# Kernel tuning notes

Measured on AMD Instinct MI355X. Metric: run time of the kernel, lower is better.

Reference implementation:

```python
import jax, jax.numpy as jnp
import numpy as np

B, N, T, D, H, E = 2, 1024, 8, 128, 4, 8192
DH = D // H
NEG_SLOPE = 0.2  # GATv2Conv default negative_slope


def _ln(x, g, b):
    m = jnp.mean(x, -1, keepdims=True)
    v = jnp.mean((x - m) ** 2, -1, keepdims=True)
    return (x - m) * jax.lax.rsqrt(v + 1e-5) * g + b


def _forward(x, edge_index, gat_wl, gat_wr, gat_att, gat_b, in_w, in_b, out_w, out_b,
             ffn_w1, ffn_b1, ffn_w2, ffn_b2, fus_w, fus_b,
             lns_g, lns_b, lnt1_g, lnt1_b, lnt2_g, lnt2_b, lnf_g, lnf_b):
    # ---- spatial branch: GATv2, vectorized over (B, T) instead of python loops ----
    loops = jnp.arange(N)
    src = jnp.concatenate([edge_index[0], loops])  # j: message source (PyG adds self loops)
    dst = jnp.concatenate([edge_index[1], loops])  # i: aggregation target
    xl = jnp.einsum('bntd,de->bnte', x, gat_wl).reshape(B, N, T, H, D)
    xr = jnp.einsum('bntd,de->bnte', x, gat_wr).reshape(B, N, T, H, D)
    ml = xl[:, src]                                  # [B,Et,T,H,D]
    mr = xr[:, dst]
    e = jax.nn.leaky_relu(ml + mr, NEG_SLOPE)
    logits = jnp.einsum('bethd,hd->beth', e, gat_att)
    logits = jnp.moveaxis(logits, 1, 0)              # [Et,B,T,H]
    mx = jax.ops.segment_max(logits, dst, num_segments=N)
    p = jnp.exp(logits - mx[dst])                    # stable edge softmax per dst node
    ssum = jax.ops.segment_sum(p, dst, num_segments=N)
    alpha = p / ssum[dst]                            # [Et,B,T,H]
    msg = alpha[..., None] * jnp.moveaxis(ml, 1, 0)
    agg = jax.ops.segment_sum(msg, dst, num_segments=N)  # [N,B,T,H,D]
    x_sp = jnp.moveaxis(agg.mean(3), 0, 1) + gat_b   # concat=False -> head mean; [B,N,T,D]
    x_sp = _ln(x_sp, lns_g, lns_b)

    # ---- temporal branch: MHA + FFN, vectorized over all B*N nodes ----
    xt = x.reshape(B * N, T, D)
    qkv = xt @ in_w + in_b
    q, k, v = jnp.split(qkv, 3, axis=-1)
    q = q.reshape(B * N, T, H, DH)
    k = k.reshape(B * N, T, H, DH)
    v = v.reshape(B * N, T, H, DH)
    scores = jnp.einsum('bthd,bshd->bhts', q, k) / np.float32(np.sqrt(DH))
    attn = jax.nn.softmax(scores, -1)
    o = jnp.einsum('bhts,bshd->bthd', attn, v).reshape(B * N, T, D)
    o = o @ out_w + out_b
    x1 = _ln(xt + o, lnt1_g, lnt1_b)
    ffn = jax.nn.gelu(x1 @ ffn_w1 + ffn_b1, approximate=False) @ ffn_w2 + ffn_b2
    x_tp = _ln(x1 + ffn, lnt2_g, lnt2_b).reshape(B, N, T, D)

    # ---- gated fusion with residual ----
    g = jax.nn.sigmoid(jnp.concatenate([x_sp, x_tp], -1) @ fus_w + fus_b)
    return _ln(g * x_sp + (1.0 - g) * x_tp + x, lnf_g, lnf_b)


def setup_inputs() -> dict:
    key = jax.random.key(0)
    ks = jax.random.split(key, 12)
    s = 0.05
    f = jnp.float32
    return {
        'x': jax.random.normal(ks[0], (B, N, T, D), f),
        'edge_index': jax.random.randint(ks[1], (2, E), 0, N),
        'gat_wl': jax.random.normal(ks[2], (D, H * D), f) * s,
        'gat_wr': jax.random.normal(ks[3], (D, H * D), f) * s,
        'gat_att': jax.random.normal(ks[4], (H, D), f) * s,
        'gat_b': jnp.zeros((D,), f),
        'in_w': jax.random.normal(ks[5], (D, 3 * D), f) * s,
        'in_b': jnp.zeros((3 * D,), f),
        'out_w': jax.random.normal(ks[6], (D, D), f) * s,
        'out_b': jnp.zeros((D,), f),
        'ffn_w1': jax.random.normal(ks[7], (D, 4 * D), f) * s,
        'ffn_b1': jnp.zeros((4 * D,), f),
        'ffn_w2': jax.random.normal(ks[8], (4 * D, D), f) * s,
        'ffn_b2': jnp.zeros((D,), f),
        'fus_w': jax.random.normal(ks[9], (2 * D, D), f) * s,
        'fus_b': jnp.zeros((D,), f),
        'lns_g': jnp.ones((D,), f), 'lns_b': jnp.zeros((D,), f),
        'lnt1_g': jnp.ones((D,), f), 'lnt1_b': jnp.zeros((D,), f),
        'lnt2_g': jnp.ones((D,), f), 'lnt2_b': jnp.zeros((D,), f),
        'lnf_g': jnp.ones((D,), f), 'lnf_b': jnp.zeros((D,), f),
    }


def reference(x, edge_index, gat_wl, gat_wr, gat_att, gat_b, in_w, in_b, out_w, out_b,
              ffn_w1, ffn_b1, ffn_w2, ffn_b2, fus_w, fus_b,
              lns_g, lns_b, lnt1_g, lnt1_b, lnt2_g, lnt2_b, lnf_g, lnf_b):
    return _forward(x, edge_index, gat_wl, gat_wr, gat_att, gat_b, in_w, in_b, out_w, out_b,
                    ffn_w1, ffn_b1, ffn_w2, ffn_b2, fus_w, fus_b,
                    lns_g, lns_b, lnt1_g, lnt1_b, lnt2_g, lnt2_b, lnf_g, lnf_b)
```

## Files before the change

### kernel.cpp

```cpp
#include <hip/hip_runtime.h>
#include <math.h>

#define B_ 2
#define N_ 1024
#define T_ 8
#define D_ 128
#define H_ 4
#define E_ 8192
#define EN_ 9216
#define M_ 16384

typedef unsigned short u16;
using bf16x8 = __attribute__((ext_vector_type(8))) short;
using f32x4  = __attribute__((ext_vector_type(4))) float;

__device__ __forceinline__ float bf2f(unsigned int u) {
  return __uint_as_float(u << 16);
}
__device__ __forceinline__ u16 f2bf(float f) {
  unsigned int x = __float_as_uint(f);
  x += 0x7fffu + ((x >> 16) & 1u);
  return (u16)(x >> 16);
}
__device__ __forceinline__ void load8f(const u16* p, float* f) {
  uint4 u = *(const uint4*)p;
  f[0]=bf2f(u.x & 0xffffu); f[1]=bf2f(u.x >> 16);
  f[2]=bf2f(u.y & 0xffffu); f[3]=bf2f(u.y >> 16);
  f[4]=bf2f(u.z & 0xffffu); f[5]=bf2f(u.z >> 16);
  f[6]=bf2f(u.w & 0xffffu); f[7]=bf2f(u.w >> 16);
}
__device__ __forceinline__ void unpack8(uint4 u, float* f) {
  f[0]=bf2f(u.x & 0xffffu); f[1]=bf2f(u.x >> 16);
  f[2]=bf2f(u.y & 0xffffu); f[3]=bf2f(u.y >> 16);
  f[4]=bf2f(u.z & 0xffffu); f[5]=bf2f(u.z >> 16);
  f[6]=bf2f(u.w & 0xffffu); f[7]=bf2f(u.w >> 16);
}
__device__ __forceinline__ void gl2lds(const u16* g, u16* l) {
  __builtin_amdgcn_global_load_lds(
      (const __attribute__((address_space(1))) unsigned int*)(const void*)g,
      (__attribute__((address_space(3))) unsigned int*)(void*)l,
      16, 0, 0);
}

__device__ __forceinline__ u16 conv_w_elem(int idx,
    const float* wl, const float* wr, const float* inw, const float* outw,
    const float* f1, const float* f2, const float* fw) {
  const float* src; int base, K, N;
  if      (idx < 65536)  { src = wl;   base = 0;      K = 128; N = 512; }
  else if (idx < 131072) { src = wr;   base = 65536;  K = 128; N = 512; }
  else if (idx < 180224) { src = inw;  base = 131072; K = 128; N = 384; }
  else if (idx < 196608) { src = outw; base = 180224; K = 128; N = 128; }
  else if (idx < 262144) { src = f1;   base = 196608; K = 128; N = 512; }
  else if (idx < 327680) { src = f2;   base = 262144; K = 512; N = 128; }
  else                   { src = fw;   base = 327680; K = 256; N = 128; }
  int o = idx - base;
  int n = o / K, k = o - n * K;
  return f2bf(src[k * N + n]);
}

__global__ __launch_bounds__(1024) void prep_csr_k(const float* __restrict__ x,
    const float* __restrict__ wl, const float* __restrict__ wr,
    const float* __restrict__ inw, const float* __restrict__ outw,
    const float* __restrict__ f1, const float* __restrict__ f2,
    const float* __restrict__ fw,
    u16* __restrict__ XB, u16* __restrict__ WB,
    const int* __restrict__ ei, int* __restrict__ offs, int* __restrict__ srcs) {
  __shared__ int cnt[N_];
  __shared__ int cur[N_];
  int bi = blockIdx.x;
  int tid = threadIdx.x;
  if (bi < 512) {
    int i = (bi * 1024 + tid) * 4;
    float4 v = *(const float4*)&x[i];
    u16 o[4] = {f2bf(v.x), f2bf(v.y), f2bf(v.z), f2bf(v.w)};
    *(ushort4*)&XB[i] = *(ushort4*)o;
    return;
  }
  if (bi < 600) {
    int base = (bi - 512) * 4096 + tid * 4;
#pragma unroll
    for (int j = 0; j < 4; ++j)
      WB[base + j] = conv_w_elem(base + j, wl, wr, inw, outw, f1, f2, fw);
    return;
  }
  cnt[tid] = 0;
  __syncthreads();
  for (int e = tid; e < EN_; e += 1024) {
    int d = (e < E_) ? ei[E_ + e] : (e - E_);
    atomicAdd(&cnt[d], 1);
  }
  __syncthreads();
  int mine = cnt[tid];
  for (int off = 1; off < 1024; off <<= 1) {
    int tv = (tid >= off) ? cnt[tid - off] : 0;
    __syncthreads();
    cnt[tid] += tv;
    __syncthreads();
  }
  int excl = cnt[tid] - mine;
  offs[tid] = excl;
  if (tid == 1023) offs[N_] = cnt[1023];
  cur[tid] = excl;
  __syncthreads();
  for (int e = tid; e < EN_; e += 1024) {
    int d = (e < E_) ? ei[E_ + e] : (e - E_);
    int s = (e < E_) ? ei[e] : (e - E_);
    int pos = atomicAdd(&cur[d], 1);
    srcs[pos] = s;
  }
}

template<int BM, int ACT, int ROUTE>
__global__ __launch_bounds__(256) void gemm_k(const u16* __restrict__ A, int lda,
                                              const u16* __restrict__ WT, int K,
                                              const float* __restrict__ bias,
                                              u16* __restrict__ C, int ldc,
                                              u16* __restrict__ R0,
                                              u16* __restrict__ R1,
                                              u16* __restrict__ R2,
                                              const float* __restrict__ b2) {
  constexpr int MI = BM / 32;
  __shared__ u16 As[BM * 32];
  __shared__ u16 Bs[128 * 32];
  int tid = threadIdx.x;
  int bx = blockIdx.x, by = blockIdx.y;
  int lane = tid & 63, wid = tid >> 6;
  int lr = lane & 15, lk = lane >> 4;
  int wm = (wid >> 1) * (BM / 2);
  int wn = (wid & 1) * 64;

  u16* Cb; int ldc_; int col0; const float* bias_;
  if (ROUTE) {
    if (bx < 4)      { Cb = R0; ldc_ = 512; col0 = bx * 128;       bias_ = nullptr; }
    else if (bx < 8) { Cb = R1; ldc_ = 512; col0 = (bx - 4) * 128; bias_ = nullptr; }
    else             { Cb = R2; ldc_ = 384; col0 = (bx - 8) * 128; bias_ = b2; }
  } else { Cb = C; ldc_ = ldc; col0 = bx * 128; bias_ = bias; }

  f32x4 acc[MI][4] = {};
  for (int k0 = 0; k0 < K; k0 += 32) {
    __syncthreads();
#pragma unroll
    for (int i = 0; i < BM / 64; ++i) {
      int o = tid * 16 + i * 4096;
      int row = o >> 6;
      int col = (o >> 1) & 31;
      gl2lds(A + (size_t)(by * BM + row) * lda + k0 + col,
             (u16*)((char*)As + wid * 1024 + i * 4096));
    }
#pragma unroll
    for (int i = 0; i < 2; ++i) {
      int o = tid * 16 + i * 4096;
      int nrow = o >> 6;
      int col = (o >> 1) & 31;
      gl2lds(WT + (size_t)(bx * 128 + nrow) * K + k0 + col,
             (u16*)((char*)Bs + wid * 1024 + i * 4096));
    }
    __syncthreads();
    bf16x8 bf[4];
#pragma unroll
    for (int ni = 0; ni < 4; ++ni)
      bf[ni] = *(const bf16x8*)&Bs[(wn + ni * 16 + lr) * 32 + lk * 8];
#pragma unroll
    for (int mi = 0; mi < MI; ++mi) {
      bf16x8 af = *(const bf16x8*)&As[(wm + mi * 16 + lr) * 32 + lk * 8];
#pragma unroll
      for (int ni = 0; ni < 4; ++ni)
        acc[mi][ni] = __builtin_amdgcn_mfma_f32_16x16x32_bf16(af, bf[ni], acc[mi][ni], 0, 0, 0);
    }
  }
  float bc[4];
#pragma unroll
  for (int ni = 0; ni < 4; ++ni)
    bc[ni] = bias_ ? bias_[col0 + wn + ni * 16 + lr] : 0.f;
#pragma unroll
  for (int mi = 0; mi < MI; ++mi) {
#pragma unroll
    for (int r = 0; r < 4; ++r) {
      int row = by * BM + wm + mi * 16 + lk * 4 + r;
#pragma unroll
      for (int ni = 0; ni < 4; ++ni) {
        int col = col0 + wn + ni * 16 + lr;
        float v = acc[mi][ni][r] + bc[ni];
        if (ACT) v = 0.5f * v * (1.f + erff(v * 0.70710678118f));
        Cb[(size_t)row * ldc_ + col] = f2bf(v);
      }
    }
  }
}

template<int EPI>
__global__ __launch_bounds__(256) void gemm_ln_k(const u16* __restrict__ A, int lda,
                                                 const u16* __restrict__ WT, int K,
                                                 const float* __restrict__ bias,
                                                 const float* __restrict__ xres,
                                                 const u16* __restrict__ xcat,
                                                 const float* __restrict__ lng,
                                                 const float* __restrict__ lnb,
                                                 float* __restrict__ o32,
                                                 u16* __restrict__ o16, int os16) {
  __shared__ u16 As[64 * 32];
  __shared__ u16 Bs[128 * 32];
  __shared__ float rs[64][2], rq[64][2];
  int tid = threadIdx.x;
  int by = blockIdx.y;
  int lane = tid & 63, wid = tid >> 6;
  int lr = lane & 15, lk = lane >> 4;
  int wm = (wid >> 1) * 32, wn = (wid & 1) * 64;

  f32x4 acc[2][4] = {};
  for (int k0 = 0; k0 < K; k0 += 32) {
    __syncthreads();
    {
      int o = tid * 16;
      int row = o >> 6;
      int col = (o >> 1) & 31;
      gl2lds(A + (size_t)(by * 64 + row) * lda + k0 + col,
             (u16*)((char*)As + wid * 1024));
    }
#pragma unroll
    for (int i = 0; i < 2; ++i) {
      int o = tid * 16 + i * 4096;
      int nrow = o >> 6;
      int col = (o >> 1) & 31;
      gl2lds(WT + (size_t)nrow * K + k0 + col,
             (u16*)((char*)Bs + wid * 1024 + i * 4096));
    }
    __syncthreads();
    bf16x8 bf[4];
#pragma unroll
    for (int ni = 0; ni < 4; ++ni)
      bf[ni] = *(const bf16x8*)&Bs[(wn + ni * 16 + lr) * 32 + lk * 8];
#pragma unroll
    for (int mi = 0; mi < 2; ++mi) {
      bf16x8 af = *(const bf16x8*)&As[(wm + mi * 16 + lr) * 32 + lk * 8];
#pragma unroll
      for (int ni = 0; ni < 4; ++ni)
        acc[mi][ni] = __builtin_amdgcn_mfma_f32_16x16x32_bf16(af, bf[ni], acc[mi][ni], 0, 0, 0);
    }
  }
  float bc[4];
#pragma unroll
  for (int ni = 0; ni < 4; ++ni) bc[ni] = bias[wn + ni * 16 + lr];

#pragma unroll
  for (int mi = 0; mi < 2; ++mi) {
#pragma unroll
    for (int r = 0; r < 4; ++r) {
      int row = by * 64 + wm + mi * 16 + lk * 4 + r;
      float s = 0.f, s2 = 0.f;
#pragma unroll
      for (int ni = 0; ni < 4; ++ni) {
        int col = wn + ni * 16 + lr;
        float v = acc[mi][ni][r] + bc[ni];
        if (EPI == 1 || EPI == 2) {
          v += xres[(size_t)row * 128 + col];
        } else {
          float gg = 1.f / (1.f + __expf(-v));
          float xsp = bf2f(xcat[(size_t)row * 256 + col]);
          float xtp = bf2f(xcat[(size_t)row * 256 + 128 + col]);
          v = gg * xsp + (1.f - gg) * xtp + xres[(size_t)row * 128 + col];
        }
        acc[mi][ni][r] = v;
        s += v; s2 += v * v;
      }
      s += __shfl_xor(s, 1, 64); s2 += __shfl_xor(s2, 1, 64);
      s += __shfl_xor(s, 2, 64); s2 += __shfl_xor(s2, 2, 64);
      s += __shfl_xor(s, 4, 64); s2 += __shfl_xor(s2, 4, 64);
      s += __shfl_xor(s, 8, 64); s2 += __shfl_xor(s2, 8, 64);
      if (lr == 0) {
        int rl = wm + mi * 16 + lk * 4 + r;
        rs[rl][wid & 1] = s;
        rq[rl][wid & 1] = s2;
      }
    }
  }
  __syncthreads();
#pragma unroll
  for (int mi = 0; mi < 2; ++mi) {
#pragma unroll
    for (int r = 0; r < 4; ++r) {
      int rl = wm + mi * 16 + lk * 4 + r;
      int row = by * 64 + rl;
      float tot = rs[rl][0] + rs[rl][1];
      float tq = rq[rl][0] + rq[rl][1];
      float mean = tot * (1.f / 128.f);
      float var = tq * (1.f / 128.f) - mean * mean;
      float rinv = rsqrtf(var + 1e-5f);
#pragma unroll
      for (int ni = 0; ni < 4; ++ni) {
        int col = wn + ni * 16 + lr;
        float o = (acc[mi][ni][r] - mean) * rinv * lng[col] + lnb[col];
        if (EPI != 2) o32[(size_t)row * 128 + col] = o;
        if (EPI != 3) o16[(size_t)row * os16 + col] = f2bf(o);
      }
    }
  }
}

__global__ __launch_bounds__(256) void gat_attn_k(const u16* __restrict__ XL,
                                                  const u16* __restrict__ XR,
                                                  const int* __restrict__ offs,
                                                  const int* __restrict__ srcs,
                                                  const float* __restrict__ att,
                                                  const float* __restrict__ gb,
                                                  const float* __restrict__ lng,
                                                  const float* __restrict__ lnb,
                                                  u16* __restrict__ XCAT,
                                                  const u16* __restrict__ QKV,
                                                  u16* __restrict__ OATT) {
  int bid = blockIdx.x;
  int wid = threadIdx.x >> 6;
  int lane = threadIdx.x & 63;
  if (bid < 4096) {
    int w = bid * 4 + wid;
    int n = w >> 4;
    int b = (w >> 3) & 1;
    int t = w & 7;
    int dd = (lane & 15) * 8;
    size_t tokn = (size_t)(b * N_ + n) * 8 + t;
    size_t rowoff = (size_t)b * (N_ * 8) + t;

    float mr[8], av[8];
    load8f(XR + tokn * 512 + lane * 8, mr);
    *(float4*)&av[0] = *(const float4*)(att + lane * 8);
    *(float4*)&av[4] = *(const float4*)(att + lane * 8 + 4);

    int beg = offs[n], end = offs[n + 1];
    float sH = 0.f;
    float acc[8] = {0.f, 0.f, 0.f, 0.f, 0.f, 0.f, 0.f, 0.f};
    int src0 = srcs[beg];
    uint4 raw_next = *(const uint4*)(XL + (rowoff + (size_t)src0 * 8) * 512 + lane * 8);
    for (int i = beg; i < end; ++i) {
      uint4 raw = raw_next;
      if (i + 1 < end) {
        int sn = srcs[i + 1];
        raw_next = *(const uint4*)(XL + (rowoff + (size_t)sn * 8) * 512 + lane * 8);
      }
      float ml[8];
      unpack8(raw, ml);
      float d = 0.f;
#pragma unroll
      for (int j = 0; j < 8; ++j) {
        float m = ml[j] + mr[j];
        m = fmaxf(m, 0.2f * m);
        d += m * av[j];
      }
      d += __shfl_xor(d, 1, 64);
      d += __shfl_xor(d, 2, 64);
      d += __shfl_xor(d, 4, 64);
      d += __shfl_xor(d, 8, 64);
      float p = __expf(d);
      sH += p;
#pragma unroll
      for (int j = 0; j < 8; ++j) acc[j] += p * ml[j];
    }
    float invS = 1.f / sH;
#pragma unroll
    for (int j = 0; j < 8; ++j) acc[j] *= invS;
#pragma unroll
    for (int j = 0; j < 8; ++j) {
      acc[j] += __shfl_xor(acc[j], 16, 64);
      acc[j] += __shfl_xor(acc[j], 32, 64);
    }
#pragma unroll
    for (int j = 0; j < 8; ++j) acc[j] = acc[j] * 0.25f + gb[dd + j];
    float s = 0.f, s2 = 0.f;
#pragma unroll
    for (int j = 0; j < 8; ++j) { s += acc[j]; s2 += acc[j] * acc[j]; }
#pragma unroll
    for (int m = 1; m < 16; m <<= 1) {
      s += __shfl_xor(s, m, 64);
      s2 += __shfl_xor(s2, m, 64);
    }
    float mean = s * (1.f / 128.f);
    float var = s2 * (1.f / 128.f) - mean * mean;
    float r = rsqrtf(var + 1e-5f);
    if (lane < 16) {
      u16 ob[8];
#pragma unroll
      for (int j = 0; j < 8; ++j)
        ob[j] = f2bf((acc[j] - mean) * r * lng[dd + j] + lnb[dd + j]);
      *(uint4*)&XCAT[tokn * 256 + dd] = *(uint4*)ob;
    }
    return;
  }
  int pair = (bid - 4096) * 4 + wid;
  int bn = pair >> 2, h = pair & 3;
  int t = lane >> 3, sidx = lane & 7;
  int dg = lane & 7;
  const u16* base = QKV + (size_t)bn * 8 * 384;
  float va[8][4];
#pragma unroll
  for (int s2 = 0; s2 < 8; ++s2) {
    ushort4 vv = *(const ushort4*)(base + s2 * 384 + 256 + h * 32 + dg * 4);
    va[s2][0] = bf2f(vv.x); va[s2][1] = bf2f(vv.y);
    va[s2][2] = bf2f(vv.z); va[s2][3] = bf2f(vv.w);
  }
  const u16* qp = base + t * 384 + h * 32;
  const u16* kp = base + sidx * 384 + 128 + h * 32;
  float sc = 0.f;
#pragma unroll
  for (int d0 = 0; d0 < 32; d0 += 8) {
    float q[8], k[8];
    load8f(qp + d0, q);
    load8f(kp + d0, k);
#pragma unroll
    for (int j = 0; j < 8; ++j) sc += q[j] * k[j];
  }
  sc *= 0.17677669529663687f;
  float m = sc;
  m = fmaxf(m, __shfl_xor(m, 1, 64));
  m = fmaxf(m, __shfl_xor(m, 2, 64));
  m = fmaxf(m, __shfl_xor(m, 4, 64));
  float p = __expf(sc - m);
  float S = p;
  S += __shfl_xor(S, 1, 64);
  S += __shfl_xor(S, 2, 64);
  S += __shfl_xor(S, 4, 64);
  float alpha = p / S;
  int tbase = lane & 56;
  float o0 = 0.f, o1 = 0.f, o2 = 0.f, o3 = 0.f;
#pragma unroll
  for (int s2 = 0; s2 < 8; ++s2) {
    float a = __shfl(alpha, tbase + s2, 64);
    o0 += a * va[s2][0];
    o1 += a * va[s2][1];
    o2 += a * va[s2][2];
    o3 += a * va[s2][3];
  }
  u16 ov[4] = {f2bf(o0), f2bf(o1), f2bf(o2), f2bf(o3)};
  *(ushort4*)&OATT[((size_t)bn * 8 + t) * 128 + h * 32 + dg * 4] = *(ushort4*)ov;
}

extern "C" void kernel_launch(void* const* d_in, const int* in_sizes, int n_in,
                              void* d_out, int out_size, void* d_ws, size_t ws_size,
                              hipStream_t stream) {
  const float* x       = (const float*)d_in[0];
  const int*   ei      = (const int*)d_in[1];
  const float* gat_att = (const float*)d_in[4];
  const float* gat_b   = (const float*)d_in[5];
  const float* in_b    = (const float*)d_in[7];
  const float* out_b   = (const float*)d_in[9];
  const float* ffn_b1  = (const float*)d_in[11];
  const float* ffn_b2  = (const float*)d_in[13];
  const float* fus_b   = (const float*)d_in[15];
  const float* lns_g   = (const float*)d_in[16];
  const float* lns_b   = (const float*)d_in[17];
  const float* lnt1_g  = (const float*)d_in[18];
  const float* lnt1_b  = (const float*)d_in[19];
  const float* lnt2_g  = (const float*)d_in[20];
  const float* lnt2_b  = (const float*)d_in[21];
  const float* lnf_g   = (const float*)d_in[22];
  const float* lnf_b   = (const float*)d_in[23];

  char* ws = (char*)d_ws;
  u16*   WB    = (u16*)ws;
  u16*   WT1   = WB;
  u16*   WTO   = WB + 180224;
  u16*   WTF1  = WB + 196608;
  u16*   WTF2  = WB + 262144;
  u16*   WTFUS = WB + 327680;
  int*   OFFS  = (int*)(ws + 3145728);
  int*   SRCS  = (int*)(ws + 3153920);
  u16*   XB   = (u16*)(ws + 4194304);
  u16*   OATT = XB;
  u16*   XL   = (u16*)(ws + 8388608);
  u16*   FFNH = XL;
  u16*   XR   = (u16*)(ws + 25165824);
  float* X1   = (float*)(ws + 33554432);
  u16*   QKV  = (u16*)(ws + 41943040);
  u16*   X1B  = (u16*)(ws + 41943040);
  u16*   XCAT = (u16*)(ws + 62914560);

  prep_csr_k<<<dim3(601), dim3(1024), 0, stream>>>(x,
      (const float*)d_in[2], (const float*)d_in[3], (const float*)d_in[6],
      (const float*)d_in[8], (const float*)d_in[10], (const float*)d_in[12],
      (const float*)d_in[14], XB, WB, ei, OFFS, SRCS);

  gemm_k<128,0,1><<<dim3(11, 128), dim3(256), 0, stream>>>(
      XB, 128, WT1, 128, nullptr, nullptr, 0, XL, XR, QKV, in_b);

  gat_attn_k<<<dim3(6144), dim3(256), 0, stream>>>(XL, XR, OFFS, SRCS,
      gat_att, gat_b, lns_g, lns_b, XCAT, QKV, OATT);

  gemm_ln_k<1><<<dim3(1, 256), dim3(256), 0, stream>>>(
      OATT, 128, WTO, 128, out_b, x, nullptr, lnt1_g, lnt1_b, X1, X1B, 128);

  gemm_k<128,1,0><<<dim3(4, 128), dim3(256), 0, stream>>>(
      X1B, 128, WTF1, 128, ffn_b1, FFNH, 512, nullptr, nullptr, nullptr, nullptr);

  gemm_ln_k<2><<<dim3(1, 256), dim3(256), 0, stream>>>(
      FFNH, 512, WTF2, 512, ffn_b2, X1, nullptr, lnt2_g, lnt2_b,
      nullptr, XCAT + 128, 256);

  gemm_ln_k<3><<<dim3(1, 256), dim3(256), 0, stream>>>(
      XCAT, 256, WTFUS, 256, fus_b, x, XCAT, lnf_g, lnf_b,
      (float*)d_out, nullptr, 0);
}
```

Before: 223.2 us.

## Fuse temporal attention into out-proj GEMM and co-schedule GAT with FFN1

Temporal MHA is now computed per block directly into shared memory and consumed by the output-projection GEMM plus LayerNorm in one kernel, removing the OATT round trip and one launch. The GAT aggregation moves out of the attention kernel and shares a launch with the FFN1 GEMM, so the irregular gather overlaps with MFMA work. Workspace buffers are re-laid out to avoid aliasing now that stages run in a different order. This costs more shared memory per block in the fused attention kernel and gives heterogeneous blocks in one grid.

```diff
diff --git a/kernel.cpp b/kernel.cpp
--- a/kernel.cpp
+++ b/kernel.cpp
@@ -111,19 +111,12 @@
 }
 
 template<int BM, int ACT, int ROUTE>
-__global__ __launch_bounds__(256) void gemm_k(const u16* __restrict__ A, int lda,
-                                              const u16* __restrict__ WT, int K,
-                                              const float* __restrict__ bias,
-                                              u16* __restrict__ C, int ldc,
-                                              u16* __restrict__ R0,
-                                              u16* __restrict__ R1,
-                                              u16* __restrict__ R2,
-                                              const float* __restrict__ b2) {
+__device__ __forceinline__ void gemm_tile(int bx, int by,
+    const u16* A, int lda, const u16* WT, int K, const float* bias,
+    u16* C, int ldc, u16* R0, u16* R1, u16* R2, const float* b2,
+    u16* As, u16* Bs) {
   constexpr int MI = BM / 32;
-  __shared__ u16 As[BM * 32];
-  __shared__ u16 Bs[128 * 32];
   int tid = threadIdx.x;
-  int bx = blockIdx.x, by = blockIdx.y;
   int lane = tid & 63, wid = tid >> 6;
   int lr = lane & 15, lk = lane >> 4;
   int wm = (wid >> 1) * (BM / 2);
@@ -189,59 +182,17 @@
 }
 
 template<int EPI>
-__global__ __launch_bounds__(256) void gemm_ln_k(const u16* __restrict__ A, int lda,
-                                                 const u16* __restrict__ WT, int K,
-                                                 const float* __restrict__ bias,
-                                                 const float* __restrict__ xres,
-                                                 const u16* __restrict__ xcat,
-                                                 const float* __restrict__ lng,
-                                                 const float* __restrict__ lnb,
-                                                 float* __restrict__ o32,
-                                                 u16* __restrict__ o16, int os16) {
-  __shared__ u16 As[64 * 32];
-  __shared__ u16 Bs[128 * 32];
-  __shared__ float rs[64][2], rq[64][2];
+__device__ __forceinline__ void ln_epilogue(int by, f32x4 (&acc)[2][4],
+    const float* bias, const float* xres, const u16* xcat,
+    const float* lng, const float* lnb,
+    float* o32, u16* o16, int os16, float* rs, float* rq) {
   int tid = threadIdx.x;
-  int by = blockIdx.y;
   int lane = tid & 63, wid = tid >> 6;
   int lr = lane & 15, lk = lane >> 4;
   int wm = (wid >> 1) * 32, wn = (wid & 1) * 64;
-
-  f32x4 acc[2][4] = {};
-  for (int k0 = 0; k0 < K; k0 += 32) {
-    __syncthreads();
-    {
-      int o = tid * 16;
-      int row = o >> 6;
-      int col = (o >> 1) & 31;
-      gl2lds(A + (size_t)(by * 64 + row) * lda + k0 + col,
-             (u16*)((char*)As + wid * 1024));
-    }
-#pragma unroll
-    for (int i = 0; i < 2; ++i) {
-      int o = tid * 16 + i * 4096;
-      int nrow = o >> 6;
-      int col = (o >> 1) & 31;
-      gl2lds(WT + (size_t)nrow * K + k0 + col,
-             (u16*)((char*)Bs + wid * 1024 + i * 4096));
-    }
-    __syncthreads();
-    bf16x8 bf[4];
-#pragma unroll
-    for (int ni = 0; ni < 4; ++ni)
-      bf[ni] = *(const bf16x8*)&Bs[(wn + ni * 16 + lr) * 32 + lk * 8];
-#pragma unroll
-    for (int mi = 0; mi < 2; ++mi) {
-      bf16x8 af = *(const bf16x8*)&As[(wm + mi * 16 + lr) * 32 + lk * 8];
-#pragma unroll
-      for (int ni = 0; ni < 4; ++ni)
-        acc[mi][ni] = __builtin_amdgcn_mfma_f32_16x16x32_bf16(af, bf[ni], acc[mi][ni], 0, 0, 0);
-    }
-  }
   float bc[4];
 #pragma unroll
   for (int ni = 0; ni < 4; ++ni) bc[ni] = bias[wn + ni * 16 + lr];
-
 #pragma unroll
   for (int mi = 0; mi < 2; ++mi) {
 #pragma unroll
@@ -269,8 +220,8 @@
       s += __shfl_xor(s, 8, 64); s2 += __shfl_xor(s2, 8, 64);
       if (lr == 0) {
         int rl = wm + mi * 16 + lk * 4 + r;
-        rs[rl][wid & 1] = s;
-        rq[rl][wid & 1] = s2;
+        rs[rl * 2 + (wid & 1)] = s;
+        rq[rl * 2 + (wid & 1)] = s2;
       }
     }
   }
@@ -281,8 +232,8 @@
     for (int r = 0; r < 4; ++r) {
       int rl = wm + mi * 16 + lk * 4 + r;
       int row = by * 64 + rl;
-      float tot = rs[rl][0] + rs[rl][1];
-      float tq = rq[rl][0] + rq[rl][1];
+      float tot = rs[rl * 2] + rs[rl * 2 + 1];
+      float tq = rq[rl * 2] + rq[rl * 2 + 1];
       float mean = tot * (1.f / 128.f);
       float var = tq * (1.f / 128.f) - mean * mean;
       float rinv = rsqrtf(var + 1e-5f);
@@ -297,139 +248,251 @@
   }
 }
 
-__global__ __launch_bounds__(256) void gat_attn_k(const u16* __restrict__ XL,
-                                                  const u16* __restrict__ XR,
-                                                  const int* __restrict__ offs,
-                                                  const int* __restrict__ srcs,
-                                                  const float* __restrict__ att,
-                                                  const float* __restrict__ gb,
-                                                  const float* __restrict__ lng,
-                                                  const float* __restrict__ lnb,
-                                                  u16* __restrict__ XCAT,
-                                                  const u16* __restrict__ QKV,
-                                                  u16* __restrict__ OATT) {
+template<int EPI>
+__global__ __launch_bounds__(256) void gemm_ln_k(const u16* __restrict__ A, int lda,
+    const u16* __restrict__ WT, int K, const float* __restrict__ bias,
+    const float* __restrict__ xres, const u16* __restrict__ xcat,
+    const float* __restrict__ lng, const float* __restrict__ lnb,
+    float* __restrict__ o32, u16* __restrict__ o16, int os16) {
+  __shared__ u16 As[64 * 32];
+  __shared__ u16 Bs[128 * 32];
+  __shared__ float rs[128], rq[128];
+  int by = blockIdx.x;
+  int tid = threadIdx.x;
+  int lane = tid & 63, wid = tid >> 6;
+  int lr = lane & 15, lk = lane >> 4;
+  int wm = (wid >> 1) * 32, wn = (wid & 1) * 64;
+
+  f32x4 acc[2][4] = {};
+  for (int k0 = 0; k0 < K; k0 += 32) {
+    __syncthreads();
+    {
+      int o = tid * 16;
+      int row = o >> 6;
+      int col = (o >> 1) & 31;
+      gl2lds(A + (size_t)(by * 64 + row) * lda + k0 + col,
+             (u16*)((char*)As + wid * 1024));
+    }
+#pragma unroll
+    for (int i = 0; i < 2; ++i) {
+      int o = tid * 16 + i * 4096;
+      int nrow = o >> 6;
+      int col = (o >> 1) & 31;
+      gl2lds(WT + (size_t)nrow * K + k0 + col,
+             (u16*)((char*)Bs + wid * 1024 + i * 4096));
+    }
+    __syncthreads();
+    bf16x8 bf[4];
+#pragma unroll
+    for (int ni = 0; ni < 4; ++ni)
+      bf[ni] = *(const bf16x8*)&Bs[(wn + ni * 16 + lr) * 32 + lk * 8];
+#pragma unroll
+    for (int mi = 0; mi < 2; ++mi) {
+      bf16x8 af = *(const bf16x8*)&As[(wm + mi * 16 + lr) * 32 + lk * 8];
+#pragma unroll
+      for (int ni = 0; ni < 4; ++ni)
+        acc[mi][ni] = __builtin_amdgcn_mfma_f32_16x16x32_bf16(af, bf[ni], acc[mi][ni], 0, 0, 0);
+    }
+  }
+  ln_epilogue<EPI>(by, acc, bias, xres, xcat, lng, lnb, o32, o16, os16, rs, rq);
+}
+
+__global__ __launch_bounds__(256) void proj_k(const u16* __restrict__ XB,
+    const u16* __restrict__ WT1, const float* __restrict__ in_b,
+    u16* __restrict__ XL, u16* __restrict__ XR, u16* __restrict__ QKV) {
+  __shared__ u16 As[128 * 32];
+  __shared__ u16 Bs[128 * 32];
+  gemm_tile<128, 0, 1>(blockIdx.x, blockIdx.y, XB, 128, WT1, 128, nullptr,
+                       nullptr, 0, XL, XR, QKV, in_b, As, Bs);
+}
+
+__global__ __launch_bounds__(256) void attn_oproj_k(const u16* __restrict__ QKV,
+    const u16* __restrict__ WTO, const float* __restrict__ out_b,
+    const float* __restrict__ x,
+    const float* __restrict__ lnt1_g, const float* __restrict__ lnt1_b,
+    float* __restrict__ X1, u16* __restrict__ X1B) {
+  __shared__ u16 As[4 * 64 * 32];
+  __shared__ u16 Bs[4 * 128 * 32];
+  __shared__ float rs[128], rq[128];
+  int by = blockIdx.x;
+  int tid = threadIdx.x;
+  int lane = tid & 63, wid = tid >> 6;
+
+#pragma unroll
+  for (int i = 0; i < 8; ++i) {
+    int o = tid * 16 + i * 4096;
+    int c = o >> 13;
+    int wb = o & 8191;
+    int nrow = wb >> 6;
+    int kin = (wb & 63) >> 1;
+    gl2lds(WTO + (size_t)nrow * 128 + c * 32 + kin,
+           (u16*)((char*)Bs + wid * 1024 + i * 4096));
+  }
+
+  int t = lane >> 3, sidx = lane & 7, dg = lane & 7;
+  for (int it = 0; it < 8; ++it) {
+    int task = wid * 8 + it;
+    int bnl = task >> 2, h = task & 3;
+    int bn = by * 8 + bnl;
+    const u16* base = QKV + (size_t)bn * 8 * 384;
+    float va[8][4];
+#pragma unroll
+    for (int s2 = 0; s2 < 8; ++s2) {
+      ushort4 vv = *(const ushort4*)(base + s2 * 384 + 256 + h * 32 + dg * 4);
+      va[s2][0] = bf2f(vv.x); va[s2][1] = bf2f(vv.y);
+      va[s2][2] = bf2f(vv.z); va[s2][3] = bf2f(vv.w);
+    }
+    const u16* qp = base + t * 384 + h * 32;
+    const u16* kp = base + sidx * 384 + 128 + h * 32;
+    float sc = 0.f;
+#pragma unroll
+    for (int d0 = 0; d0 < 32; d0 += 8) {
+      float q[8], k[8];
+      load8f(qp + d0, q);
+      load8f(kp + d0, k);
+#pragma unroll
+      for (int j = 0; j < 8; ++j) sc += q[j] * k[j];
+    }
+    sc *= 0.17677669529663687f;
+    float m = sc;
+    m = fmaxf(m, __shfl_xor(m, 1, 64));
+    m = fmaxf(m, __shfl_xor(m, 2, 64));
+    m = fmaxf(m, __shfl_xor(m, 4, 64));
+    float p = __expf(sc - m);
+    float S = p;
+    S += __shfl_xor(S, 1, 64);
+    S += __shfl_xor(S, 2, 64);
+    S += __shfl_xor(S, 4, 64);
+    float alpha = p / S;
+    int tb = lane & 56;
+    float o0 = 0.f, o1 = 0.f, o2 = 0.f, o3 = 0.f;
+#pragma unroll
+    for (int s2 = 0; s2 < 8; ++s2) {
+      float a = __shfl(alpha, tb + s2, 64);
+      o0 += a * va[s2][0];
+      o1 += a * va[s2][1];
+      o2 += a * va[s2][2];
+      o3 += a * va[s2][3];
+    }
+    u16 ov[4] = {f2bf(o0), f2bf(o1), f2bf(o2), f2bf(o3)};
+    int row = bnl * 8 + t;
+    *(ushort4*)&As[h * 2048 + row * 32 + dg * 4] = *(ushort4*)ov;
+  }
+  __syncthreads();
+
+  int lr = lane & 15, lk = lane >> 4;
+  int wm = (wid >> 1) * 32, wn = (wid & 1) * 64;
+  f32x4 acc[2][4] = {};
+#pragma unroll
+  for (int c = 0; c < 4; ++c) {
+    bf16x8 bf[4];
+#pragma unroll
+    for (int ni = 0; ni < 4; ++ni)
+      bf[ni] = *(const bf16x8*)&Bs[c * 4096 + (wn + ni * 16 + lr) * 32 + lk * 8];
+#pragma unroll
+    for (int mi = 0; mi < 2; ++mi) {
+      bf16x8 af = *(const bf16x8*)&As[c * 2048 + (wm + mi * 16 + lr) * 32 + lk * 8];
+#pragma unroll
+      for (int ni = 0; ni < 4; ++ni)
+        acc[mi][ni] = __builtin_amdgcn_mfma_f32_16x16x32_bf16(af, bf[ni], acc[mi][ni], 0, 0, 0);
+    }
+  }
+  ln_epilogue<1>(by, acc, out_b, x, nullptr, lnt1_g, lnt1_b, X1, X1B, 128, rs, rq);
+}
+
+__device__ __forceinline__ void gat_wave(int w, int lane,
+    const u16* XL, const u16* XR, const int* offs, const int* srcs,
+    const float* att, const float* gb, const float* lng, const float* lnb,
+    u16* XCAT) {
+  int n = w >> 4;
+  int b = (w >> 3) & 1;
+  int t = w & 7;
+  int dd = (lane & 15) * 8;
+  size_t tokn = (size_t)(b * N_ + n) * 8 + t;
+  size_t rowoff = (size_t)b * (N_ * 8) + t;
+
+  float mr[8], av[8];
+  load8f(XR + tokn * 512 + lane * 8, mr);
+  *(float4*)&av[0] = *(const float4*)(att + lane * 8);
+  *(float4*)&av[4] = *(const float4*)(att + lane * 8 + 4);
+
+  int beg = offs[n], end = offs[n + 1];
+  float sH = 0.f;
+  float acc[8] = {0.f, 0.f, 0.f, 0.f, 0.f, 0.f, 0.f, 0.f};
+  int src0 = srcs[beg];
+  uint4 raw_next = *(const uint4*)(XL + (rowoff + (size_t)src0 * 8) * 512 + lane * 8);
+  for (int i = beg; i < end; ++i) {
+    uint4 raw = raw_next;
+    if (i + 1 < end) {
+      int sn = srcs[i + 1];
+      raw_next = *(const uint4*)(XL + (rowoff + (size_t)sn * 8) * 512 + lane * 8);
+    }
+    float ml[8];
+    unpack8(raw, ml);
+    float d = 0.f;
+#pragma unroll
+    for (int j = 0; j < 8; ++j) {
+      float m = ml[j] + mr[j];
+      m = fmaxf(m, 0.2f * m);
+      d += m * av[j];
+    }
+    d += __shfl_xor(d, 1, 64);
+    d += __shfl_xor(d, 2, 64);
+    d += __shfl_xor(d, 4, 64);
+    d += __shfl_xor(d, 8, 64);
+    float p = __expf(d);
+    sH += p;
+#pragma unroll
+    for (int j = 0; j < 8; ++j) acc[j] += p * ml[j];
+  }
+  float invS = 1.f / sH;
+#pragma unroll
+  for (int j = 0; j < 8; ++j) acc[j] *= invS;
+#pragma unroll
+  for (int j = 0; j < 8; ++j) {
+    acc[j] += __shfl_xor(acc[j], 16, 64);
+    acc[j] += __shfl_xor(acc[j], 32, 64);
+  }
+#pragma unroll
+  for (int j = 0; j < 8; ++j) acc[j] = acc[j] * 0.25f + gb[dd + j];
+  float s = 0.f, s2 = 0.f;
+#pragma unroll
+  for (int j = 0; j < 8; ++j) { s += acc[j]; s2 += acc[j] * acc[j]; }
+#pragma unroll
+  for (int m = 1; m < 16; m <<= 1) {
+    s += __shfl_xor(s, m, 64);
+    s2 += __shfl_xor(s2, m, 64);
+  }
+  float mean = s * (1.f / 128.f);
+  float var = s2 * (1.f / 128.f) - mean * mean;
+  float r = rsqrtf(var + 1e-5f);
+  if (lane < 16) {
+    u16 ob[8];
+#pragma unroll
+    for (int j = 0; j < 8; ++j)
+      ob[j] = f2bf((acc[j] - mean) * r * lng[dd + j] + lnb[dd + j]);
+    *(uint4*)&XCAT[tokn * 256 + dd] = *(uint4*)ob;
+  }
+}
+
+__global__ __launch_bounds__(256) void ffn1_gat_k(const u16* __restrict__ X1B,
+    const u16* __restrict__ WTF1, const float* __restrict__ ffn_b1,
+    u16* __restrict__ FFNH,
+    const u16* __restrict__ XL, const u16* __restrict__ XR,
+    const int* __restrict__ offs, const int* __restrict__ srcs,
+    const float* __restrict__ att, const float* __restrict__ gb,
+    const float* __restrict__ lng, const float* __restrict__ lnb,
+    u16* __restrict__ XCAT) {
+  __shared__ u16 As[128 * 32];
+  __shared__ u16 Bs[128 * 32];
   int bid = blockIdx.x;
-  int wid = threadIdx.x >> 6;
-  int lane = threadIdx.x & 63;
-  if (bid < 4096) {
-    int w = bid * 4 + wid;
-    int n = w >> 4;
-    int b = (w >> 3) & 1;
-    int t = w & 7;
-    int dd = (lane & 15) * 8;
-    size_t tokn = (size_t)(b * N_ + n) * 8 + t;
-    size_t rowoff = (size_t)b * (N_ * 8) + t;
-
-    float mr[8], av[8];
-    load8f(XR + tokn * 512 + lane * 8, mr);
-    *(float4*)&av[0] = *(const float4*)(att + lane * 8);
-    *(float4*)&av[4] = *(const float4*)(att + lane * 8 + 4);
-
-    int beg = offs[n], end = offs[n + 1];
-    float sH = 0.f;
-    float acc[8] = {0.f, 0.f, 0.f, 0.f, 0.f, 0.f, 0.f, 0.f};
-    int src0 = srcs[beg];
-    uint4 raw_next = *(const uint4*)(XL + (rowoff + (size_t)src0 * 8) * 512 + lane * 8);
-    for (int i = beg; i < end; ++i) {
-      uint4 raw = raw_next;
-      if (i + 1 < end) {
-        int sn = srcs[i + 1];
-        raw_next = *(const uint4*)(XL + (rowoff + (size_t)sn * 8) * 512 + lane * 8);
-      }
-      float ml[8];
-      unpack8(raw, ml);
-      float d = 0.f;
-#pragma unroll
-      for (int j = 0; j < 8; ++j) {
-        float m = ml[j] + mr[j];
-        m = fmaxf(m, 0.2f * m);
-        d += m * av[j];
-      }
-      d += __shfl_xor(d, 1, 64);
-      d += __shfl_xor(d, 2, 64);
-      d += __shfl_xor(d, 4, 64);
-      d += __shfl_xor(d, 8, 64);
-      float p = __expf(d);
-      sH += p;
-#pragma unroll
-      for (int j = 0; j < 8; ++j) acc[j] += p * ml[j];
-    }
-    float invS = 1.f / sH;
-#pragma unroll
-    for (int j = 0; j < 8; ++j) acc[j] *= invS;
-#pragma unroll
-    for (int j = 0; j < 8; ++j) {
-      acc[j] += __shfl_xor(acc[j], 16, 64);
-      acc[j] += __shfl_xor(acc[j], 32, 64);
-    }
-#pragma unroll
-    for (int j = 0; j < 8; ++j) acc[j] = acc[j] * 0.25f + gb[dd + j];
-    float s = 0.f, s2 = 0.f;
-#pragma unroll
-    for (int j = 0; j < 8; ++j) { s += acc[j]; s2 += acc[j] * acc[j]; }
-#pragma unroll
-    for (int m = 1; m < 16; m <<= 1) {
-      s += __shfl_xor(s, m, 64);
-      s2 += __shfl_xor(s2, m, 64);
-    }
-    float mean = s * (1.f / 128.f);
-    float var = s2 * (1.f / 128.f) - mean * mean;
-    float r = rsqrtf(var + 1e-5f);
-    if (lane < 16) {
-      u16 ob[8];
-#pragma unroll
-      for (int j = 0; j < 8; ++j)
-        ob[j] = f2bf((acc[j] - mean) * r * lng[dd + j] + lnb[dd + j]);
-      *(uint4*)&XCAT[tokn * 256 + dd] = *(uint4*)ob;
-    }
-    return;
-  }
-  int pair = (bid - 4096) * 4 + wid;
-  int bn = pair >> 2, h = pair & 3;
-  int t = lane >> 3, sidx = lane & 7;
-  int dg = lane & 7;
-  const u16* base = QKV + (size_t)bn * 8 * 384;
-  float va[8][4];
-#pragma unroll
-  for (int s2 = 0; s2 < 8; ++s2) {
-    ushort4 vv = *(const ushort4*)(base + s2 * 384 + 256 + h * 32 + dg * 4);
-    va[s2][0] = bf2f(vv.x); va[s2][1] = bf2f(vv.y);
-    va[s2][2] = bf2f(vv.z); va[s2][3] = bf2f(vv.w);
-  }
-  const u16* qp = base + t * 384 + h * 32;
-  const u16* kp = base + sidx * 384 + 128 + h * 32;
-  float sc = 0.f;
-#pragma unroll
-  for (int d0 = 0; d0 < 32; d0 += 8) {
-    float q[8], k[8];
-    load8f(qp + d0, q);
-    load8f(kp + d0, k);
-#pragma unroll
-    for (int j = 0; j < 8; ++j) sc += q[j] * k[j];
-  }
-  sc *= 0.17677669529663687f;
-  float m = sc;
-  m = fmaxf(m, __shfl_xor(m, 1, 64));
-  m = fmaxf(m, __shfl_xor(m, 2, 64));
-  m = fmaxf(m, __shfl_xor(m, 4, 64));
-  float p = __expf(sc - m);
-  float S = p;
-  S += __shfl_xor(S, 1, 64);
-  S += __shfl_xor(S, 2, 64);
-  S += __shfl_xor(S, 4, 64);
-  float alpha = p / S;
-  int tbase = lane & 56;
-  float o0 = 0.f, o1 = 0.f, o2 = 0.f, o3 = 0.f;
-#pragma unroll
-  for (int s2 = 0; s2 < 8; ++s2) {
-    float a = __shfl(alpha, tbase + s2, 64);
-    o0 += a * va[s2][0];
-    o1 += a * va[s2][1];
-    o2 += a * va[s2][2];
-    o3 += a * va[s2][3];
-  }
-  u16 ov[4] = {f2bf(o0), f2bf(o1), f2bf(o2), f2bf(o3)};
-  *(ushort4*)&OATT[((size_t)bn * 8 + t) * 128 + h * 32 + dg * 4] = *(ushort4*)ov;
+  if (bid < 512) {
+    gemm_tile<128, 1, 0>(bid >> 7, bid & 127, X1B, 128, WTF1, 128, ffn_b1,
+                         FFNH, 512, nullptr, nullptr, nullptr, nullptr, As, Bs);
+  } else {
+    gat_wave((bid - 512) * 4 + (threadIdx.x >> 6), threadIdx.x & 63,
+             XL, XR, offs, srcs, att, gb, lng, lnb, XCAT);
+  }
 }
 
 extern "C" void kernel_launch(void* const* d_in, const int* in_sizes, int n_in,
@@ -455,7 +518,6 @@
 
   char* ws = (char*)d_ws;
   u16*   WB    = (u16*)ws;
-  u16*   WT1   = WB;
   u16*   WTO   = WB + 180224;
   u16*   WTF1  = WB + 196608;
   u16*   WTF2  = WB + 262144;
@@ -463,37 +525,30 @@
   int*   OFFS  = (int*)(ws + 3145728);
   int*   SRCS  = (int*)(ws + 3153920);
   u16*   XB   = (u16*)(ws + 4194304);
-  u16*   OATT = XB;
   u16*   XL   = (u16*)(ws + 8388608);
-  u16*   FFNH = XL;
   u16*   XR   = (u16*)(ws + 25165824);
-  float* X1   = (float*)(ws + 33554432);
-  u16*   QKV  = (u16*)(ws + 41943040);
-  u16*   X1B  = (u16*)(ws + 41943040);
-  u16*   XCAT = (u16*)(ws + 62914560);
+  float* X1   = (float*)(ws + 41943040);
+  u16*   QKV  = (u16*)(ws + 50331648);
+  u16*   X1B  = (u16*)(ws + 62914560);
+  u16*   FFNH = (u16*)(ws + 67108864);
+  u16*   XCAT = (u16*)(ws + 83886080);
 
   prep_csr_k<<<dim3(601), dim3(1024), 0, stream>>>(x,
       (const float*)d_in[2], (const float*)d_in[3], (const float*)d_in[6],
       (const float*)d_in[8], (const float*)d_in[10], (const float*)d_in[12],
       (const float*)d_in[14], XB, WB, ei, OFFS, SRCS);
 
-  gemm_k<128,0,1><<<dim3(11, 128), dim3(256), 0, stream>>>(
-      XB, 128, WT1, 128, nullptr, nullptr, 0, XL, XR, QKV, in_b);
-
-  gat_attn_k<<<dim3(6144), dim3(256), 0, stream>>>(XL, XR, OFFS, SRCS,
-      gat_att, gat_b, lns_g, lns_b, XCAT, QKV, OATT);
-
-  gemm_ln_k<1><<<dim3(1, 256), dim3(256), 0, stream>>>(
-      OATT, 128, WTO, 128, out_b, x, nullptr, lnt1_g, lnt1_b, X1, X1B, 128);
-
-  gemm_k<128,1,0><<<dim3(4, 128), dim3(256), 0, stream>>>(
-      X1B, 128, WTF1, 128, ffn_b1, FFNH, 512, nullptr, nullptr, nullptr, nullptr);
-
-  gemm_ln_k<2><<<dim3(1, 256), dim3(256), 0, stream>>>(
-      FFNH, 512, WTF2, 512, ffn_b2, X1, nullptr, lnt2_g, lnt2_b,
-      nullptr, XCAT + 128, 256);
-
-  gemm_ln_k<3><<<dim3(1, 256), dim3(256), 0, stream>>>(
-      XCAT, 256, WTFUS, 256, fus_b, x, XCAT, lnf_g, lnf_b,
-      (float*)d_out, nullptr, 0);
-}
+  proj_k<<<dim3(11, 128), dim3(256), 0, stream>>>(XB, WB, in_b, XL, XR, QKV);
+
+  attn_oproj_k<<<dim3(256), dim3(256), 0, stream>>>(QKV, WTO, out_b, x,
+      lnt1_g, lnt1_b, X1, X1B);
+
+  ffn1_gat_k<<<dim3(4608), dim3(256), 0, stream>>>(X1B, WTF1, ffn_b1, FFNH,
+      XL, XR, OFFS, SRCS, gat_att, gat_b, lns_g, lns_b, XCAT);
+
+  gemm_ln_k<2><<<dim3(256), dim3(256), 0, stream>>>(FFNH, 512, WTF2, 512,
+      ffn_b2, X1, nullptr, lnt2_g, lnt2_b, nullptr, XCAT + 128, 256);
+
+  gemm_ln_k<3><<<dim3(256), dim3(256), 0, stream>>>(XCAT, 256, WTFUS, 256,
+      fus_b, x, XCAT, lnf_g, lnf_b, (float*)d_out, nullptr, 0);
+}
```

Result: slower. 228.5 us (+2.4%).
